# Optimization experiments

Hardware: AMD Instinct MI355X
Metric: run time of the kernel (lower is better)

The kernel has to match this reference:

```python
import jax, jax.numpy as jnp
import numpy as np

D = 256
H = 8
DIM = D // H
NL = 8  # number of layers
LAYER_NAMES = ["self", "cross", "self", "cross", "self", "cross", "self", "cross"]
EPS_ATTN = 1e-6
EPS_LN = 1e-5


def setup_inputs() -> dict:
    key = jax.random.key(0)
    ks = jax.random.split(key, 16)
    B, L = 8, 4800
    s = 1.0 / np.sqrt(D)
    inp = {
        "desc0": jax.random.normal(ks[0], (B, L, D), jnp.float32),
        "desc1": jax.random.normal(ks[1], (B, L, D), jnp.float32),
        "mask0": jnp.ones((B, L), jnp.float32),
        "mask1": jnp.ones((B, L), jnp.float32),
        # shared LinearAttention params (one instance reused by all layers)
        "Wq": jax.random.normal(ks[2], (D, D), jnp.float32) * s,
        "bq": jnp.zeros((D,), jnp.float32),
        "Wk": jax.random.normal(ks[3], (D, D), jnp.float32) * s,
        "bk": jnp.zeros((D,), jnp.float32),
        "Wv": jax.random.normal(ks[4], (D, D), jnp.float32) * s,
        "bv": jnp.zeros((D,), jnp.float32),
        "Wm": jax.random.normal(ks[5], (D, D), jnp.float32) * s,
        "bm": jnp.zeros((D,), jnp.float32),
        # per-layer MLP (no bias) and layernorm params, stacked over layers
        "w1": jax.random.normal(ks[6], (NL, D, 2 * D), jnp.float32) * s,
        "w2": jax.random.normal(ks[7], (NL, 2 * D, D), jnp.float32) * (1.0 / np.sqrt(2 * D)),
        "g1": jnp.ones((NL, D), jnp.float32),
        "b1": jnp.zeros((NL, D), jnp.float32),
        "g2": jnp.ones((NL, D), jnp.float32),
        "b2": jnp.zeros((NL, D), jnp.float32),
    }
    return inp


def _layernorm(x, g, b):
    mu = jnp.mean(x, axis=-1, keepdims=True)
    var = jnp.mean(jnp.square(x - mu), axis=-1, keepdims=True)
    return (x - mu) * jax.lax.rsqrt(var + EPS_LN) * g + b


def _linear_attention(q_in, k_in, v_in, qmask, kmask, Wq, bq, Wk, bk, Wv, bv, Wm, bm):
    B, L, _ = q_in.shape
    Q = (q_in @ Wq + bq).reshape(B, -1, H, DIM)
    K = (k_in @ Wk + bk).reshape(B, -1, H, DIM)
    V = (v_in @ Wv + bv).reshape(B, -1, H, DIM)
    Q = jax.nn.elu(Q) + 1.0
    K = jax.nn.elu(K) + 1.0
    Q = Q * qmask[:, :, None, None]
    K = K * kmask[:, :, None, None]
    V = V * kmask[:, :, None, None]
    KV = jnp.einsum("nshd,nshm->nhmd", K, V)          # [B,H,DIM,DIM]
    Z = 1.0 / (jnp.einsum("nlhd,nhd->nlh", Q, K.sum(axis=1)) + EPS_ATTN)
    out = jnp.einsum("nlhd,nhmd,nlh->nlhm", Q, KV, Z)  # [B,L,H,DIM]
    return out.reshape(B, L, D) @ Wm + bm


def _layer(x, source, xmask, smask, Wq, bq, Wk, bk, Wv, bv, Wm, bm, w1, w2, g1, b1, g2, b2):
    msg = _linear_attention(x, source, source, xmask, smask, Wq, bq, Wk, bk, Wv, bv, Wm, bm)
    msg = _layernorm(msg, g1, b1)
    msg = jax.nn.relu(msg @ w1) @ w2
    msg = _layernorm(msg, g2, b2)
    return x + msg


def reference(desc0, desc1, mask0, mask1, Wq, bq, Wk, bk, Wv, bv, Wm, bm, w1, w2, g1, b1, g2, b2):
    attn = (Wq, bq, Wk, bk, Wv, bv, Wm, bm)
    for i, name in enumerate(LAYER_NAMES):
        lp = (w1[i], w2[i], g1[i], b1[i], g2[i], b2[i])
        if name == "self":
            desc0 = _layer(desc0, desc0, mask0, mask0, *attn, *lp)
            desc1 = _layer(desc1, desc1, mask1, mask1, *attn, *lp)
        else:
            desc0 = _layer(desc0, desc1, mask0, mask1, *attn, *lp)
            desc1 = _layer(desc1, desc0, mask1, mask0, *attn, *lp)
    return (desc0, desc1)
```

## Files before the change

### kernel.cpp

```cpp
#include <hip/hip_runtime.h>
#include <hip/hip_bf16.h>

typedef __attribute__((ext_vector_type(8))) short short8;
typedef __attribute__((ext_vector_type(4))) float f32x4;

#define NROWS 38400
#define LSEQ 4800
#define BATCH 8
#define NHEAD 8
#define QKV_LD 768

__device__ inline float b2f(ushort u) {
  union { ushort s; __hip_bfloat16 h; } c;
  c.s = u;
  return __bfloat162float(c.h);
}
__device__ inline ushort f2b(float f) {
  union { ushort s; __hip_bfloat16 h; } c;
  c.h = __float2bfloat16(f);
  return c.s;
}

__device__ inline void gll16(const void* g, void* l) {
  __builtin_amdgcn_global_load_lds(
      (const __attribute__((address_space(1))) void*)g,
      (__attribute__((address_space(3))) void*)l, 16, 0, 0);
}

__global__ __launch_bounds__(256) void transpose_bf16(
    const float* __restrict__ src, __hip_bfloat16* __restrict__ dst, int R, int C) {
  src += (size_t)blockIdx.z * R * C;
  dst += (size_t)blockIdx.z * R * C;
  __shared__ float tile[32][33];
  int bx = blockIdx.x, by = blockIdx.y;
  int tx = threadIdx.x & 31, ty = threadIdx.x >> 5;
  for (int rr = ty; rr < 32; rr += 8)
    tile[rr][tx] = src[(long)(by * 32 + rr) * C + bx * 32 + tx];
  __syncthreads();
  for (int rr = ty; rr < 32; rr += 8)
    dst[(long)(bx * 32 + rr) * R + by * 32 + tx] = __float2bfloat16(tile[tx][rr]);
}

__global__ __launch_bounds__(256) void init_x(
    const float* __restrict__ d0, const float* __restrict__ d1,
    float* __restrict__ outF, __hip_bfloat16* __restrict__ X0b,
    __hip_bfloat16* __restrict__ X1b, long n4) {
  long i = (long)blockIdx.x * 256 + threadIdx.x;
  if (i < n4) {
    float4 a = ((const float4*)d0)[i];
    float4 b = ((const float4*)d1)[i];
    ((float4*)outF)[i] = a;
    ((float4*)outF)[n4 + i] = b;
    ushort4 ua = {f2b(a.x), f2b(a.y), f2b(a.z), f2b(a.w)};
    ushort4 ub = {f2b(b.x), f2b(b.y), f2b(b.z), f2b(b.w)};
    ((ushort4*)X0b)[i] = ua;
    ((ushort4*)X1b)[i] = ub;
  }
}

__global__ __launch_bounds__(256) void gemm_qkv(
    const __hip_bfloat16* __restrict__ A, const __hip_bfloat16* __restrict__ Bt,
    __hip_bfloat16* __restrict__ C, int col0,
    const float* __restrict__ bq, const float* __restrict__ bk,
    const float* __restrict__ bv, const float* __restrict__ mq,
    const float* __restrict__ mkv) {
  __shared__ alignas(16) char smem[128 * 136 * 2];
  __hip_bfloat16 (*As)[64] = (__hip_bfloat16(*)[64])smem;
  __hip_bfloat16 (*Bs)[64] = (__hip_bfloat16(*)[64])(smem + 128 * 64 * 2);
  ushort (*Cs)[136] = (ushort(*)[136])smem;

  int tid = threadIdx.x;
  int wave = tid >> 6, lane = tid & 63;
  int wm = wave & 1, wn = wave >> 1;
  int quad = lane >> 4, l16 = lane & 15;
  long mbase = (long)blockIdx.y * 128;
  int nbase = blockIdx.x * 128;

  int srow = lane >> 3;
  int sck = (lane & 7) ^ srow;
  int cx = l16 & 7;

  f32x4 acc[4][4];
#pragma unroll
  for (int i = 0; i < 4; i++)
#pragma unroll
    for (int j = 0; j < 4; j++) acc[i][j] = (f32x4){0.f, 0.f, 0.f, 0.f};

  for (int kt = 0; kt < 256; kt += 64) {
    __syncthreads();
#pragma unroll
    for (int i = 0; i < 4; i++) {
      int r0 = wave * 32 + i * 8;
      gll16(A + (mbase + r0 + srow) * 256 + kt + sck * 8, &As[r0][0]);
      gll16(Bt + (long)(nbase + r0 + srow) * 256 + kt + sck * 8, &Bs[r0][0]);
    }
    __syncthreads();
#pragma unroll
    for (int ks = 0; ks < 64; ks += 32) {
      short8 af[4], bfr[4];
      int ch = ((ks >> 3) + quad) ^ cx;
#pragma unroll
      for (int mt = 0; mt < 4; mt++)
        af[mt] = *(const short8*)&As[wm * 64 + mt * 16 + l16][ch * 8];
#pragma unroll
      for (int nt = 0; nt < 4; nt++)
        bfr[nt] = *(const short8*)&Bs[wn * 64 + nt * 16 + l16][ch * 8];
#pragma unroll
      for (int mt = 0; mt < 4; mt++)
#pragma unroll
        for (int nt = 0; nt < 4; nt++)
          acc[mt][nt] = __builtin_amdgcn_mfma_f32_16x16x32_bf16(
              af[mt], bfr[nt], acc[mt][nt], 0, 0, 0);
    }
  }

  __syncthreads();
  int gc0 = col0 + nbase;
#pragma unroll
  for (int nt = 0; nt < 4; nt++) {
    int colt = wn * 64 + nt * 16 + l16;
    int gcol = gc0 + colt;
    int seg = gcol >> 8;
    int ci = gcol & 255;
    float bvv = (seg == 0) ? bq[ci] : (seg == 1) ? bk[ci] : bv[ci];
    const float* mask = (seg == 0) ? mq : mkv;
    bool doelu = seg < 2;
#pragma unroll
    for (int mt = 0; mt < 4; mt++) {
      int rowt0 = wm * 64 + mt * 16 + quad * 4;
#pragma unroll
      for (int r = 0; r < 4; r++) {
        int rowt = rowt0 + r;
        float v = acc[mt][nt][r] + bvv;
        if (doelu) v = v > 0.f ? v + 1.f : __expf(v);
        v *= mask[mbase + rowt];
        Cs[rowt][colt] = f2b(v);
      }
    }
  }
  __syncthreads();
#pragma unroll
  for (int it = 0; it < 8; it++) {
    int idx = tid + it * 256;
    int row = idx >> 4, c = idx & 15;
    uint4 v = *(const uint4*)&Cs[row][c * 8];
    *(uint4*)(C + (mbase + row) * (long)QKV_LD + gc0 + c * 8) = v;
  }
}

__global__ __launch_bounds__(256) void gemm_w1(
    const __hip_bfloat16* __restrict__ A, const __hip_bfloat16* __restrict__ Bt,
    __hip_bfloat16* __restrict__ C) {
  __shared__ alignas(16) char smem[128 * 136 * 2];
  __hip_bfloat16 (*As)[64] = (__hip_bfloat16(*)[64])smem;
  __hip_bfloat16 (*Bs)[64] = (__hip_bfloat16(*)[64])(smem + 128 * 64 * 2);
  ushort (*Cs)[136] = (ushort(*)[136])smem;

  int tid = threadIdx.x;
  int wave = tid >> 6, lane = tid & 63;
  int wm = wave & 1, wn = wave >> 1;
  int quad = lane >> 4, l16 = lane & 15;
  long mbase = (long)blockIdx.y * 128;
  int nbase = blockIdx.x * 128;

  int srow = lane >> 3;
  int sck = (lane & 7) ^ srow;
  int cx = l16 & 7;

  f32x4 acc[4][4];
#pragma unroll
  for (int i = 0; i < 4; i++)
#pragma unroll
    for (int j = 0; j < 4; j++) acc[i][j] = (f32x4){0.f, 0.f, 0.f, 0.f};

  for (int kt = 0; kt < 256; kt += 64) {
    __syncthreads();
#pragma unroll
    for (int i = 0; i < 4; i++) {
      int r0 = wave * 32 + i * 8;
      gll16(A + (mbase + r0 + srow) * 256 + kt + sck * 8, &As[r0][0]);
      gll16(Bt + (long)(nbase + r0 + srow) * 256 + kt + sck * 8, &Bs[r0][0]);
    }
    __syncthreads();
#pragma unroll
    for (int ks = 0; ks < 64; ks += 32) {
      short8 af[4], bfr[4];
      int ch = ((ks >> 3) + quad) ^ cx;
#pragma unroll
      for (int mt = 0; mt < 4; mt++)
        af[mt] = *(const short8*)&As[wm * 64 + mt * 16 + l16][ch * 8];
#pragma unroll
      for (int nt = 0; nt < 4; nt++)
        bfr[nt] = *(const short8*)&Bs[wn * 64 + nt * 16 + l16][ch * 8];
#pragma unroll
      for (int mt = 0; mt < 4; mt++)
#pragma unroll
        for (int nt = 0; nt < 4; nt++)
          acc[mt][nt] = __builtin_amdgcn_mfma_f32_16x16x32_bf16(
              af[mt], bfr[nt], acc[mt][nt], 0, 0, 0);
    }
  }

  __syncthreads();
#pragma unroll
  for (int nt = 0; nt < 4; nt++) {
    int colt = wn * 64 + nt * 16 + l16;
#pragma unroll
    for (int mt = 0; mt < 4; mt++) {
      int rowt0 = wm * 64 + mt * 16 + quad * 4;
#pragma unroll
      for (int r = 0; r < 4; r++) {
        float v = acc[mt][nt][r];
        Cs[rowt0 + r][colt] = f2b(v > 0.f ? v : 0.f);
      }
    }
  }
  __syncthreads();
#pragma unroll
  for (int it = 0; it < 8; it++) {
    int idx = tid + it * 256;
    int row = idx >> 4, c = idx & 15;
    uint4 v = *(const uint4*)&Cs[row][c * 8];
    *(uint4*)(C + (mbase + row) * 512L + nbase + c * 8) = v;
  }
}

__global__ __launch_bounds__(256) void gemm_ln(
    const __hip_bfloat16* __restrict__ A, const __hip_bfloat16* __restrict__ Bt,
    const float* __restrict__ bias, const float* __restrict__ g,
    const float* __restrict__ bln, __hip_bfloat16* __restrict__ C) {
  __shared__ alignas(16) char smem[8192 + 32768];
  __hip_bfloat16 (*As)[64] = (__hip_bfloat16(*)[64])smem;
  __hip_bfloat16 (*Bs)[64] = (__hip_bfloat16(*)[64])(smem + 8192);
  ushort (*Cs)[264] = (ushort(*)[264])smem;
  float* pS  = (float*)(smem + 33792);
  float* pS2 = (float*)(smem + 34816);
  float* muA = (float*)(smem + 35840);
  float* rsA = (float*)(smem + 36096);

  int tid = threadIdx.x;
  int wave = tid >> 6, lane = tid & 63;
  int wn = wave;
  int quad = lane >> 4, l16 = lane & 15;
  long mbase = (long)blockIdx.x * 64;

  int srow = lane >> 3;
  int sck = (lane & 7) ^ srow;
  int cx = l16 & 7;

  f32x4 acc[4][4];
#pragma unroll
  for (int i = 0; i < 4; i++)
#pragma unroll
    for (int j = 0; j < 4; j++) acc[i][j] = (f32x4){0.f, 0.f, 0.f, 0.f};

  for (int kt = 0; kt < 256; kt += 64) {
    __syncthreads();
#pragma unroll
    for (int j = 0; j < 2; j++) {
      int r0 = wave * 16 + j * 8;
      gll16(A + (mbase + r0 + srow) * 256 + kt + sck * 8, &As[r0][0]);
    }
#pragma unroll
    for (int j = 0; j < 8; j++) {
      int r0 = wave * 64 + j * 8;
      gll16(Bt + (r0 + srow) * 256 + kt + sck * 8, &Bs[r0][0]);
    }
    __syncthreads();
#pragma unroll
    for (int ks = 0; ks < 64; ks += 32) {
      short8 af[4], bfr[4];
      int ch = ((ks >> 3) + quad) ^ cx;
#pragma unroll
      for (int mt = 0; mt < 4; mt++)
        af[mt] = *(const short8*)&As[mt * 16 + l16][ch * 8];
#pragma unroll
      for (int nt = 0; nt < 4; nt++)
        bfr[nt] = *(const short8*)&Bs[wn * 64 + nt * 16 + l16][ch * 8];
#pragma unroll
      for (int mt = 0; mt < 4; mt++)
#pragma unroll
        for (int nt = 0; nt < 4; nt++)
          acc[mt][nt] = __builtin_amdgcn_mfma_f32_16x16x32_bf16(
              af[mt], bfr[nt], acc[mt][nt], 0, 0, 0);
    }
  }
  __syncthreads();

  float br[4], gr[4], blr[4];
#pragma unroll
  for (int nt = 0; nt < 4; nt++) {
    int gcol = wn * 64 + nt * 16 + l16;
    br[nt] = bias[gcol];
    gr[nt] = g[gcol];
    blr[nt] = bln[gcol];
  }
#pragma unroll
  for (int mt = 0; mt < 4; mt++)
#pragma unroll
    for (int r = 0; r < 4; r++) {
      float s = 0.f, s2 = 0.f;
#pragma unroll
      for (int nt = 0; nt < 4; nt++) {
        float v = acc[mt][nt][r] + br[nt];
        s += v;
        s2 += v * v;
      }
      s += __shfl_xor(s, 1);  s2 += __shfl_xor(s2, 1);
      s += __shfl_xor(s, 2);  s2 += __shfl_xor(s2, 2);
      s += __shfl_xor(s, 4);  s2 += __shfl_xor(s2, 4);
      s += __shfl_xor(s, 8);  s2 += __shfl_xor(s2, 8);
      if (l16 == 0) {
        int row = mt * 16 + quad * 4 + r;
        pS[wn * 64 + row] = s;
        pS2[wn * 64 + row] = s2;
      }
    }
  __syncthreads();
  if (tid < 64) {
    float S = pS[tid] + pS[64 + tid] + pS[128 + tid] + pS[192 + tid];
    float S2 = pS2[tid] + pS2[64 + tid] + pS2[128 + tid] + pS2[192 + tid];
    float mu = S * (1.f / 256.f);
    float var = S2 * (1.f / 256.f) - mu * mu;
    muA[tid] = mu;
    rsA[tid] = rsqrtf(var + 1e-5f);
  }
  __syncthreads();
#pragma unroll
  for (int mt = 0; mt < 4; mt++)
#pragma unroll
    for (int r = 0; r < 4; r++) {
      int row = mt * 16 + quad * 4 + r;
      float mu = muA[row], rs = rsA[row];
#pragma unroll
      for (int nt = 0; nt < 4; nt++) {
        float v = acc[mt][nt][r] + br[nt];
        Cs[row][wn * 64 + nt * 16 + l16] = f2b((v - mu) * rs * gr[nt] + blr[nt]);
      }
    }
  __syncthreads();
#pragma unroll
  for (int it = 0; it < 8; it++) {
    int idx = tid + it * 256;
    int row = idx >> 5, c = idx & 31;
    uint4 v = *(const uint4*)&Cs[row][c * 8];
    *(uint4*)(C + (mbase + row) * 256L + c * 8) = v;
  }
}

__global__ __launch_bounds__(256) void gemm_final(
    const __hip_bfloat16* __restrict__ A, const __hip_bfloat16* __restrict__ Bt,
    const float* __restrict__ g, const float* __restrict__ bln,
    float* __restrict__ outF, __hip_bfloat16* __restrict__ Xb) {
  __shared__ alignas(16) char smem[8192 + 32768];
  __hip_bfloat16 (*As)[64] = (__hip_bfloat16(*)[64])smem;
  __hip_bfloat16 (*Bs)[64] = (__hip_bfloat16(*)[64])(smem + 8192);
  ushort (*Cs)[264] = (ushort(*)[264])smem;
  float* pS  = (float*)(smem + 33792);
  float* pS2 = (float*)(smem + 34816);
  float* muA = (float*)(smem + 35840);
  float* rsA = (float*)(smem + 36096);

  int tid = threadIdx.x;
  int wave = tid >> 6, lane = tid & 63;
  int wn = wave;
  int quad = lane >> 4, l16 = lane & 15;
  long mbase = (long)blockIdx.x * 64;

  int srow = lane >> 3;
  int sck = (lane & 7) ^ srow;
  int cx = l16 & 7;

  f32x4 acc[4][4];
#pragma unroll
  for (int i = 0; i < 4; i++)
#pragma unroll
    for (int j = 0; j < 4; j++) acc[i][j] = (f32x4){0.f, 0.f, 0.f, 0.f};

  for (int kt = 0; kt < 512; kt += 64) {
    __syncthreads();
#pragma unroll
    for (int j = 0; j < 2; j++) {
      int r0 = wave * 16 + j * 8;
      gll16(A + (mbase + r0 + srow) * 512 + kt + sck * 8, &As[r0][0]);
    }
#pragma unroll
    for (int j = 0; j < 8; j++) {
      int r0 = wave * 64 + j * 8;
      gll16(Bt + (r0 + srow) * 512L + kt + sck * 8, &Bs[r0][0]);
    }
    __syncthreads();
#pragma unroll
    for (int ks = 0; ks < 64; ks += 32) {
      short8 af[4], bfr[4];
      int ch = ((ks >> 3) + quad) ^ cx;
#pragma unroll
      for (int mt = 0; mt < 4; mt++)
        af[mt] = *(const short8*)&As[mt * 16 + l16][ch * 8];
#pragma unroll
      for (int nt = 0; nt < 4; nt++)
        bfr[nt] = *(const short8*)&Bs[wn * 64 + nt * 16 + l16][ch * 8];
#pragma unroll
      for (int mt = 0; mt < 4; mt++)
#pragma unroll
        for (int nt = 0; nt < 4; nt++)
          acc[mt][nt] = __builtin_amdgcn_mfma_f32_16x16x32_bf16(
              af[mt], bfr[nt], acc[mt][nt], 0, 0, 0);
    }
  }
  __syncthreads();

  float gr[4], blr[4];
#pragma unroll
  for (int nt = 0; nt < 4; nt++) {
    int gcol = wn * 64 + nt * 16 + l16;
    gr[nt] = g[gcol];
    blr[nt] = bln[gcol];
  }
#pragma unroll
  for (int mt = 0; mt < 4; mt++)
#pragma unroll
    for (int r = 0; r < 4; r++) {
      float s = 0.f, s2 = 0.f;
#pragma unroll
      for (int nt = 0; nt < 4; nt++) {
        float v = acc[mt][nt][r];
        s += v;
        s2 += v * v;
      }
      s += __shfl_xor(s, 1);  s2 += __shfl_xor(s2, 1);
      s += __shfl_xor(s, 2);  s2 += __shfl_xor(s2, 2);
      s += __shfl_xor(s, 4);  s2 += __shfl_xor(s2, 4);
      s += __shfl_xor(s, 8);  s2 += __shfl_xor(s2, 8);
      if (l16 == 0) {
        int row = mt * 16 + quad * 4 + r;
        pS[wn * 64 + row] = s;
        pS2[wn * 64 + row] = s2;
      }
    }
  __syncthreads();
  if (tid < 64) {
    float S = pS[tid] + pS[64 + tid] + pS[128 + tid] + pS[192 + tid];
    float S2 = pS2[tid] + pS2[64 + tid] + pS2[128 + tid] + pS2[192 + tid];
    float mu = S * (1.f / 256.f);
    float var = S2 * (1.f / 256.f) - mu * mu;
    muA[tid] = mu;
    rsA[tid] = rsqrtf(var + 1e-5f);
  }
  __syncthreads();
#pragma unroll
  for (int mt = 0; mt < 4; mt++)
#pragma unroll
    for (int r = 0; r < 4; r++) {
      int row = mt * 16 + quad * 4 + r;
      float mu = muA[row], rs = rsA[row];
#pragma unroll
      for (int nt = 0; nt < 4; nt++) {
        int gcol = wn * 64 + nt * 16 + l16;
        float ln = (acc[mt][nt][r] - mu) * rs * gr[nt] + blr[nt];
        float* op = outF + (mbase + row) * 256 + gcol;
        float rr = *op + ln;
        *op = rr;
        Cs[row][gcol] = f2b(rr);
      }
    }
  __syncthreads();
#pragma unroll
  for (int it = 0; it < 8; it++) {
    int idx = tid + it * 256;
    int row = idx >> 5, c = idx & 31;
    uint4 v = *(const uint4*)&Cs[row][c * 8];
    *(uint4*)(Xb + (mbase + row) * 256L + c * 8) = v;
  }
}

__global__ __launch_bounds__(256) void kv_reduce(
    const __hip_bfloat16* __restrict__ QKV, float* __restrict__ KV,
    float* __restrict__ Ksum) {
  int b = blockIdx.x, h = blockIdx.y, c = blockIdx.z;
  __shared__ float Kl[32][40], Vl[32][40];
  int t = threadIdx.x;
  int lrow = t >> 3, le = (t & 7) * 4;
  int d = t >> 3, mg = t & 7;
  float a0 = 0.f, a1 = 0.f, a2 = 0.f, a3 = 0.f, ks = 0.f;
  int base = c * 480;
  for (int st = 0; st < 15; st++) {
    int s0 = base + st * 32;
    __syncthreads();
    {
      long n = (long)b * LSEQ + s0 + lrow;
      ushort4 ku = *(const ushort4*)(QKV + n * QKV_LD + 256 + h * 32 + le);
      ushort4 vu = *(const ushort4*)(QKV + n * QKV_LD + 512 + h * 32 + le);
      float4 kf = {b2f(ku.x), b2f(ku.y), b2f(ku.z), b2f(ku.w)};
      float4 vf = {b2f(vu.x), b2f(vu.y), b2f(vu.z), b2f(vu.w)};
      *(float4*)&Kl[lrow][le] = kf;
      *(float4*)&Vl[lrow][le] = vf;
    }
    __syncthreads();
#pragma unroll
    for (int ss = 0; ss < 32; ss++) {
      float kd = Kl[ss][d];
      float4 v4 = *(const float4*)&Vl[ss][mg * 4];
      a0 += kd * v4.x; a1 += kd * v4.y; a2 += kd * v4.z; a3 += kd * v4.w;
      if (mg == 0) ks += kd;
    }
  }
  int bh = b * 8 + h;
  float* p = KV + ((long)bh * 32 + d) * 32 + mg * 4;
  atomicAdd(&p[0], a0); atomicAdd(&p[1], a1);
  atomicAdd(&p[2], a2); atomicAdd(&p[3], a3);
  if (mg == 0) atomicAdd(&Ksum[bh * 32 + d], ks);
}

__global__ __launch_bounds__(256) void attn_out(
    const __hip_bfloat16* __restrict__ QKV, const float* __restrict__ KV,
    const float* __restrict__ Ksum, __hip_bfloat16* __restrict__ O) {
  int b = blockIdx.y, h = blockIdx.z;
  int bh = b * 8 + h;
  __shared__ float KVl[32][36];
  int t = threadIdx.x;
  for (int i = t; i < 1024; i += 256) KVl[i >> 5][i & 31] = KV[((long)bh << 10) + i];
  int lane = t & 63, wave = t >> 6;
  int cg = lane & 7, rs = lane >> 3;
  float4 ksr = *(const float4*)&Ksum[bh * 32 + cg * 4];
  __syncthreads();

  int rowEnd = blockIdx.x * 192 + 192;
  for (int r = blockIdx.x * 192 + wave * 8 + rs; r < rowEnd; r += 32) {
    long n = (long)b * LSEQ + r;
    ushort4 qu = *(const ushort4*)(QKV + n * QKV_LD + h * 32 + cg * 4);
    float q0 = b2f(qu.x), q1 = b2f(qu.y), q2 = b2f(qu.z), q3 = b2f(qu.w);
    float den = q0 * ksr.x + q1 * ksr.y + q2 * ksr.z + q3 * ksr.w;
    den += __shfl_xor(den, 1);
    den += __shfl_xor(den, 2);
    den += __shfl_xor(den, 4);
    float s0 = 0.f, s1 = 0.f, s2 = 0.f, s3 = 0.f;
    int gbase = lane & ~7;
#pragma unroll
    for (int j = 0; j < 8; j++) {
      int src = gbase | j;
      float qa = __shfl(q0, src);
      float qb = __shfl(q1, src);
      float qc = __shfl(q2, src);
      float qd = __shfl(q3, src);
      float4 k0 = *(const float4*)&KVl[j * 4 + 0][cg * 4];
      float4 k1 = *(const float4*)&KVl[j * 4 + 1][cg * 4];
      float4 k2 = *(const float4*)&KVl[j * 4 + 2][cg * 4];
      float4 k3 = *(const float4*)&KVl[j * 4 + 3][cg * 4];
      s0 += qa * k0.x + qb * k1.x + qc * k2.x + qd * k3.x;
      s1 += qa * k0.y + qb * k1.y + qc * k2.y + qd * k3.y;
      s2 += qa * k0.z + qb * k1.z + qc * k2.z + qd * k3.z;
      s3 += qa * k0.w + qb * k1.w + qc * k2.w + qd * k3.w;
    }
    float inv = 1.0f / (den + 1e-6f);
    ushort4 ou = {f2b(s0 * inv), f2b(s1 * inv), f2b(s2 * inv), f2b(s3 * inv)};
    *(ushort4*)(O + n * 256 + h * 32 + cg * 4) = ou;
  }
}

extern "C" void kernel_launch(void* const* d_in, const int* in_sizes, int n_in,
                              void* d_out, int out_size, void* d_ws, size_t ws_size,
                              hipStream_t stream) {
  const float* desc0 = (const float*)d_in[0];
  const float* desc1 = (const float*)d_in[1];
  const float* mask0 = (const float*)d_in[2];
  const float* mask1 = (const float*)d_in[3];
  const float* Wq = (const float*)d_in[4];
  const float* bq = (const float*)d_in[5];
  const float* Wk = (const float*)d_in[6];
  const float* bk = (const float*)d_in[7];
  const float* Wv = (const float*)d_in[8];
  const float* bv = (const float*)d_in[9];
  const float* Wm = (const float*)d_in[10];
  const float* bm = (const float*)d_in[11];
  const float* w1 = (const float*)d_in[12];
  const float* w2 = (const float*)d_in[13];
  const float* g1 = (const float*)d_in[14];
  const float* b1 = (const float*)d_in[15];
  const float* g2 = (const float*)d_in[16];
  const float* b2 = (const float*)d_in[17];

  char* ws = (char*)d_ws;
  size_t used = 0;
  auto alloc = [&](size_t bytes) {
    char* p = ws + used;
    used += (bytes + 255) & ~(size_t)255;
    return p;
  };
  __hip_bfloat16* WqkvT = (__hip_bfloat16*)alloc((size_t)768 * 256 * 2);
  __hip_bfloat16* WmT = (__hip_bfloat16*)alloc(256 * 256 * 2);
  __hip_bfloat16* w1T = (__hip_bfloat16*)alloc((size_t)8 * 512 * 256 * 2);
  __hip_bfloat16* w2T = (__hip_bfloat16*)alloc((size_t)8 * 256 * 512 * 2);
  __hip_bfloat16* X0b = (__hip_bfloat16*)alloc((size_t)NROWS * 256 * 2);
  __hip_bfloat16* X1b = (__hip_bfloat16*)alloc((size_t)NROWS * 256 * 2);
  __hip_bfloat16* QKV = (__hip_bfloat16*)alloc((size_t)NROWS * QKV_LD * 2);
  __hip_bfloat16* Mb2 = QKV;
  __hip_bfloat16* Ab2 = (__hip_bfloat16*)alloc((size_t)2 * NROWS * 256 * 2);
  __hip_bfloat16* H1b2 = (__hip_bfloat16*)alloc((size_t)2 * NROWS * 512 * 2);
  float* KVws = (float*)alloc((64 * 1024 + 64 * 32) * 4);
  float* Ksum = KVws + 64 * 1024;
  bool merged = used <= ws_size;

  transpose_bf16<<<dim3(8, 8, 1), 256, 0, stream>>>(Wq, WqkvT, 256, 256);
  transpose_bf16<<<dim3(8, 8, 1), 256, 0, stream>>>(Wk, WqkvT + 65536, 256, 256);
  transpose_bf16<<<dim3(8, 8, 1), 256, 0, stream>>>(Wv, WqkvT + 131072, 256, 256);
  transpose_bf16<<<dim3(8, 8, 1), 256, 0, stream>>>(Wm, WmT, 256, 256);
  transpose_bf16<<<dim3(16, 8, 8), 256, 0, stream>>>(w1, w1T, 256, 512);
  transpose_bf16<<<dim3(8, 16, 8), 256, 0, stream>>>(w2, w2T, 512, 256);

  long nElem = (long)NROWS * 256;
  long n4 = nElem / 4;
  init_x<<<(n4 + 255) / 256, 256, 0, stream>>>(desc0, desc1, (float*)d_out,
                                               X0b, X1b, n4);

  auto attn_stage = [&](const __hip_bfloat16* Xq, const __hip_bfloat16* Xkv,
                        const float* mq, const float* ms,
                        __hip_bfloat16* Oout, bool self) {
    if (self) {
      gemm_qkv<<<dim3(6, 300), 256, 0, stream>>>(Xq, WqkvT, QKV, 0,
                                                 bq, bk, bv, mq, ms);
    } else {
      gemm_qkv<<<dim3(2, 300), 256, 0, stream>>>(Xq, WqkvT, QKV, 0,
                                                 bq, bk, bv, mq, ms);
      gemm_qkv<<<dim3(4, 300), 256, 0, stream>>>(Xkv, WqkvT + 65536, QKV, 256,
                                                 bq, bk, bv, mq, ms);
    }
    hipMemsetAsync(KVws, 0, (64 * 1024 + 64 * 32) * 4, stream);
    kv_reduce<<<dim3(BATCH, NHEAD, 10), 256, 0, stream>>>(QKV, KVws, Ksum);
    attn_out<<<dim3(25, BATCH, NHEAD), 256, 0, stream>>>(QKV, KVws, Ksum, Oout);
  };

  auto self_pair = [&](int i) {
    attn_stage(X0b, X0b, mask0, mask0, Ab2, true);
    attn_stage(X1b, X1b, mask1, mask1, Ab2 + nElem, true);
    gemm_ln<<<2 * NROWS / 64, 256, 0, stream>>>(Ab2, WmT, bm, g1 + i * 256,
                                                b1 + i * 256, Mb2);
    gemm_w1<<<dim3(4, 2 * NROWS / 128), 256, 0, stream>>>(
        Mb2, w1T + (size_t)i * 512 * 256, H1b2);
    gemm_final<<<2 * NROWS / 64, 256, 0, stream>>>(
        H1b2, w2T + (size_t)i * 256 * 512, g2 + i * 256, b2 + i * 256,
        (float*)d_out, X0b);
  };

  auto layer_one = [&](int x, int s, int i) {
    __hip_bfloat16* Xx = x ? X1b : X0b;
    __hip_bfloat16* Xs = s ? X1b : X0b;
    const float* mx = x ? mask1 : mask0;
    const float* ms = s ? mask1 : mask0;
    attn_stage(Xx, Xs, mx, ms, Ab2, x == s);
    gemm_ln<<<NROWS / 64, 256, 0, stream>>>(Ab2, WmT, bm, g1 + i * 256,
                                            b1 + i * 256, Mb2);
    gemm_w1<<<dim3(4, NROWS / 128), 256, 0, stream>>>(
        Mb2, w1T + (size_t)i * 512 * 256, H1b2);
    gemm_final<<<NROWS / 64, 256, 0, stream>>>(
        H1b2, w2T + (size_t)i * 256 * 512, g2 + i * 256, b2 + i * 256,
        (float*)d_out + (size_t)x * nElem, Xx);
  };

  for (int i = 0; i < 8; i++) {
    if (i % 2 == 0) {
      if (merged) {
        self_pair(i);
      } else {
        layer_one(0, 0, i);
        layer_one(1, 1, i);
      }
    } else {
      layer_one(0, 1, i);
      layer_one(1, 0, i);
    }
  }
}
```

Before: 3.331 ms.

## Double-buffer LDS tiles in gemm_ln and gemm_final to overlap loads with MFMA

The K-loop in gemm_ln and gemm_final now uses two LDS buffers. The next tile is issued with global_load_lds while MFMAs run on the current tile, and only one barrier is kept per iteration. This hides global-to-LDS load latency behind compute. In exchange, LDS use grows to 80KB per block, which may cut how many blocks fit per CU and so lower occupancy.

```diff
diff --git a/kernel.cpp b/kernel.cpp
--- a/kernel.cpp
+++ b/kernel.cpp
@@ -229,9 +229,7 @@
     const __hip_bfloat16* __restrict__ A, const __hip_bfloat16* __restrict__ Bt,
     const float* __restrict__ bias, const float* __restrict__ g,
     const float* __restrict__ bln, __hip_bfloat16* __restrict__ C) {
-  __shared__ alignas(16) char smem[8192 + 32768];
-  __hip_bfloat16 (*As)[64] = (__hip_bfloat16(*)[64])smem;
-  __hip_bfloat16 (*Bs)[64] = (__hip_bfloat16(*)[64])(smem + 8192);
+  __shared__ alignas(16) char smem[81920];
   ushort (*Cs)[264] = (ushort(*)[264])smem;
   float* pS  = (float*)(smem + 33792);
   float* pS2 = (float*)(smem + 34816);
@@ -254,8 +252,10 @@
 #pragma unroll
     for (int j = 0; j < 4; j++) acc[i][j] = (f32x4){0.f, 0.f, 0.f, 0.f};
 
-  for (int kt = 0; kt < 256; kt += 64) {
-    __syncthreads();
+  auto stage = [&](int bi, int kt) {
+    char* base = smem + bi * 40960;
+    __hip_bfloat16 (*As)[64] = (__hip_bfloat16(*)[64])base;
+    __hip_bfloat16 (*Bs)[64] = (__hip_bfloat16(*)[64])(base + 8192);
 #pragma unroll
     for (int j = 0; j < 2; j++) {
       int r0 = wave * 16 + j * 8;
@@ -266,7 +266,11 @@
       int r0 = wave * 64 + j * 8;
       gll16(Bt + (r0 + srow) * 256 + kt + sck * 8, &Bs[r0][0]);
     }
-    __syncthreads();
+  };
+  auto compute = [&](int bi) {
+    char* base = smem + bi * 40960;
+    __hip_bfloat16 (*As)[64] = (__hip_bfloat16(*)[64])base;
+    __hip_bfloat16 (*Bs)[64] = (__hip_bfloat16(*)[64])(base + 8192);
 #pragma unroll
     for (int ks = 0; ks < 64; ks += 32) {
       short8 af[4], bfr[4];
@@ -284,8 +288,20 @@
           acc[mt][nt] = __builtin_amdgcn_mfma_f32_16x16x32_bf16(
               af[mt], bfr[nt], acc[mt][nt], 0, 0, 0);
     }
-  }
-  __syncthreads();
+  };
+
+  stage(0, 0);
+  asm volatile("s_waitcnt vmcnt(0)" ::: "memory");
+  __builtin_amdgcn_sched_barrier(0);
+  __builtin_amdgcn_s_barrier();
+#pragma unroll
+  for (int t = 0; t < 4; t++) {
+    if (t + 1 < 4) stage((t + 1) & 1, (t + 1) * 64);
+    compute(t & 1);
+    asm volatile("s_waitcnt vmcnt(0)" ::: "memory");
+    __builtin_amdgcn_sched_barrier(0);
+    __builtin_amdgcn_s_barrier();
+  }
 
   float br[4], gr[4], blr[4];
 #pragma unroll
@@ -352,9 +368,7 @@
     const __hip_bfloat16* __restrict__ A, const __hip_bfloat16* __restrict__ Bt,
     const float* __restrict__ g, const float* __restrict__ bln,
     float* __restrict__ outF, __hip_bfloat16* __restrict__ Xb) {
-  __shared__ alignas(16) char smem[8192 + 32768];
-  __hip_bfloat16 (*As)[64] = (__hip_bfloat16(*)[64])smem;
-  __hip_bfloat16 (*Bs)[64] = (__hip_bfloat16(*)[64])(smem + 8192);
+  __shared__ alignas(16) char smem[81920];
   ushort (*Cs)[264] = (ushort(*)[264])smem;
   float* pS  = (float*)(smem + 33792);
   float* pS2 = (float*)(smem + 34816);
@@ -377,8 +391,10 @@
 #pragma unroll
     for (int j = 0; j < 4; j++) acc[i][j] = (f32x4){0.f, 0.f, 0.f, 0.f};
 
-  for (int kt = 0; kt < 512; kt += 64) {
-    __syncthreads();
+  auto stage = [&](int bi, int kt) {
+    char* base = smem + bi * 40960;
+    __hip_bfloat16 (*As)[64] = (__hip_bfloat16(*)[64])base;
+    __hip_bfloat16 (*Bs)[64] = (__hip_bfloat16(*)[64])(base + 8192);
 #pragma unroll
     for (int j = 0; j < 2; j++) {
       int r0 = wave * 16 + j * 8;
@@ -389,7 +405,11 @@
       int r0 = wave * 64 + j * 8;
       gll16(Bt + (r0 + srow) * 512L + kt + sck * 8, &Bs[r0][0]);
     }
-    __syncthreads();
+  };
+  auto compute = [&](int bi) {
+    char* base = smem + bi * 40960;
+    __hip_bfloat16 (*As)[64] = (__hip_bfloat16(*)[64])base;
+    __hip_bfloat16 (*Bs)[64] = (__hip_bfloat16(*)[64])(base + 8192);
 #pragma unroll
     for (int ks = 0; ks < 64; ks += 32) {
       short8 af[4], bfr[4];
@@ -407,8 +427,20 @@
           acc[mt][nt] = __builtin_amdgcn_mfma_f32_16x16x32_bf16(
               af[mt], bfr[nt], acc[mt][nt], 0, 0, 0);
     }
-  }
-  __syncthreads();
+  };
+
+  stage(0, 0);
+  asm volatile("s_waitcnt vmcnt(0)" ::: "memory");
+  __builtin_amdgcn_sched_barrier(0);
+  __builtin_amdgcn_s_barrier();
+#pragma unroll
+  for (int t = 0; t < 8; t++) {
+    if (t + 1 < 8) stage((t + 1) & 1, (t + 1) * 64);
+    compute(t & 1);
+    asm volatile("s_waitcnt vmcnt(0)" ::: "memory");
+    __builtin_amdgcn_sched_barrier(0);
+    __builtin_amdgcn_s_barrier();
+  }
 
   float gr[4], blr[4];
 #pragma unroll
```

Result: no change. 3.266 ms (-1.9%).

## Fuse output projection, LayerNorm, MLP and final LayerNorm into one kernel

Applied to the files above, without the earlier changes.

Replaces the three tail kernels (Wm GEMM + LN1, W1 GEMM + ReLU, W2 GEMM + LN2 + residual) with a single 512-thread kernel per 64-row tile. The intermediate M and H1 activations stay in swizzled shared memory instead of round-tripping through global memory. Weight tiles are double-buffered with global_load_lds prefetch of the next stage. This removes launches and large intermediate HBM traffic, at the cost of about 150KB LDS per block (one block per CU) and re-reading all weights for every row tile.

```diff
diff --git a/kernel.cpp b/kernel.cpp
--- a/kernel.cpp
+++ b/kernel.cpp
@@ -148,152 +148,154 @@
   }
 }
 
-__global__ __launch_bounds__(256) void gemm_w1(
-    const __hip_bfloat16* __restrict__ A, const __hip_bfloat16* __restrict__ Bt,
-    __hip_bfloat16* __restrict__ C) {
-  __shared__ alignas(16) char smem[128 * 136 * 2];
-  __hip_bfloat16 (*As)[64] = (__hip_bfloat16(*)[64])smem;
-  __hip_bfloat16 (*Bs)[64] = (__hip_bfloat16(*)[64])(smem + 128 * 64 * 2);
-  ushort (*Cs)[136] = (ushort(*)[136])smem;
+__global__ __launch_bounds__(512) void tail_fused(
+    const __hip_bfloat16* __restrict__ A, const __hip_bfloat16* __restrict__ WmT,
+    const __hip_bfloat16* __restrict__ w1T, const __hip_bfloat16* __restrict__ w2T,
+    const float* __restrict__ bm,
+    const float* __restrict__ g1, const float* __restrict__ b1,
+    const float* __restrict__ g2, const float* __restrict__ b2,
+    float* __restrict__ outF, __hip_bfloat16* __restrict__ Xb) {
+  __shared__ alignas(16) char smem[152064];
+  ushort* Msu  = (ushort*)(smem + 81920);
+  ushort* H1u  = (ushort*)(smem + 114688);
+  float* pS  = (float*)(smem + 147456);
+  float* pS2 = (float*)(smem + 149504);
+  float* muA = (float*)(smem + 151552);
+  float* rsA = (float*)(smem + 151808);
 
   int tid = threadIdx.x;
   int wave = tid >> 6, lane = tid & 63;
-  int wm = wave & 1, wn = wave >> 1;
   int quad = lane >> 4, l16 = lane & 15;
-  long mbase = (long)blockIdx.y * 128;
-  int nbase = blockIdx.x * 128;
-
+  long mbase = (long)blockIdx.x * 64;
   int srow = lane >> 3;
   int sck = (lane & 7) ^ srow;
   int cx = l16 & 7;
-
-  f32x4 acc[4][4];
+  int swz = cx * 8;
+
+  f32x4 accA[4][2], accB[4][2], accC[4][2];
 #pragma unroll
   for (int i = 0; i < 4; i++)
 #pragma unroll
-    for (int j = 0; j < 4; j++) acc[i][j] = (f32x4){0.f, 0.f, 0.f, 0.f};
-
-  for (int kt = 0; kt < 256; kt += 64) {
-    __syncthreads();
-#pragma unroll
-    for (int i = 0; i < 4; i++) {
-      int r0 = wave * 32 + i * 8;
-      gll16(A + (mbase + r0 + srow) * 256 + kt + sck * 8, &As[r0][0]);
-      gll16(Bt + (long)(nbase + r0 + srow) * 256 + kt + sck * 8, &Bs[r0][0]);
-    }
-    __syncthreads();
+    for (int j = 0; j < 2; j++) {
+      accA[i][j] = (f32x4){0.f, 0.f, 0.f, 0.f};
+      accC[i][j] = (f32x4){0.f, 0.f, 0.f, 0.f};
+    }
+
+  auto stageA = [&](int b, int kt) {
+    char* base = smem + b * 40960;
+    __hip_bfloat16 (*As)[64] = (__hip_bfloat16(*)[64])base;
+    __hip_bfloat16 (*Bs)[64] = (__hip_bfloat16(*)[64])(base + 8192);
+    gll16(A + (mbase + wave * 8 + srow) * 256 + kt + sck * 8, &As[wave * 8][0]);
+#pragma unroll
+    for (int j = 0; j < 4; j++) {
+      int r0 = wave * 32 + j * 8;
+      gll16(WmT + (r0 + srow) * 256 + kt + sck * 8, &Bs[r0][0]);
+    }
+  };
+  auto stageB = [&](int b, int half, int kt) {
+    __hip_bfloat16 (*Bs)[64] = (__hip_bfloat16(*)[64])(smem + b * 40960 + 8192);
+#pragma unroll
+    for (int j = 0; j < 4; j++) {
+      int r0 = wave * 32 + j * 8;
+      gll16(w1T + (half * 256 + r0 + srow) * 256 + kt + sck * 8, &Bs[r0][0]);
+    }
+  };
+  auto stageC = [&](int b, int half, int kt) {
+    __hip_bfloat16 (*Bs)[64] = (__hip_bfloat16(*)[64])(smem + b * 40960 + 8192);
+#pragma unroll
+    for (int j = 0; j < 4; j++) {
+      int r0 = wave * 32 + j * 8;
+      gll16(w2T + (r0 + srow) * 512L + half * 256 + kt + sck * 8, &Bs[r0][0]);
+    }
+  };
+
+  auto computeA = [&](int b) {
+    char* base = smem + b * 40960;
+    __hip_bfloat16 (*As)[64] = (__hip_bfloat16(*)[64])base;
+    __hip_bfloat16 (*Bs)[64] = (__hip_bfloat16(*)[64])(base + 8192);
 #pragma unroll
     for (int ks = 0; ks < 64; ks += 32) {
-      short8 af[4], bfr[4];
+      short8 af[4], bfr[2];
       int ch = ((ks >> 3) + quad) ^ cx;
 #pragma unroll
       for (int mt = 0; mt < 4; mt++)
-        af[mt] = *(const short8*)&As[wm * 64 + mt * 16 + l16][ch * 8];
-#pragma unroll
-      for (int nt = 0; nt < 4; nt++)
-        bfr[nt] = *(const short8*)&Bs[wn * 64 + nt * 16 + l16][ch * 8];
-#pragma unroll
-      for (int mt = 0; mt < 4; mt++)
-#pragma unroll
-        for (int nt = 0; nt < 4; nt++)
-          acc[mt][nt] = __builtin_amdgcn_mfma_f32_16x16x32_bf16(
-              af[mt], bfr[nt], acc[mt][nt], 0, 0, 0);
-    }
-  }
-
-  __syncthreads();
-#pragma unroll
-  for (int nt = 0; nt < 4; nt++) {
-    int colt = wn * 64 + nt * 16 + l16;
-#pragma unroll
-    for (int mt = 0; mt < 4; mt++) {
-      int rowt0 = wm * 64 + mt * 16 + quad * 4;
-#pragma unroll
-      for (int r = 0; r < 4; r++) {
-        float v = acc[mt][nt][r];
-        Cs[rowt0 + r][colt] = f2b(v > 0.f ? v : 0.f);
-      }
-    }
-  }
-  __syncthreads();
-#pragma unroll
-  for (int it = 0; it < 8; it++) {
-    int idx = tid + it * 256;
-    int row = idx >> 4, c = idx & 15;
-    uint4 v = *(const uint4*)&Cs[row][c * 8];
-    *(uint4*)(C + (mbase + row) * 512L + nbase + c * 8) = v;
-  }
-}
-
-__global__ __launch_bounds__(256) void gemm_ln(
-    const __hip_bfloat16* __restrict__ A, const __hip_bfloat16* __restrict__ Bt,
-    const float* __restrict__ bias, const float* __restrict__ g,
-    const float* __restrict__ bln, __hip_bfloat16* __restrict__ C) {
-  __shared__ alignas(16) char smem[8192 + 32768];
-  __hip_bfloat16 (*As)[64] = (__hip_bfloat16(*)[64])smem;
-  __hip_bfloat16 (*Bs)[64] = (__hip_bfloat16(*)[64])(smem + 8192);
-  ushort (*Cs)[264] = (ushort(*)[264])smem;
-  float* pS  = (float*)(smem + 33792);
-  float* pS2 = (float*)(smem + 34816);
-  float* muA = (float*)(smem + 35840);
-  float* rsA = (float*)(smem + 36096);
-
-  int tid = threadIdx.x;
-  int wave = tid >> 6, lane = tid & 63;
-  int wn = wave;
-  int quad = lane >> 4, l16 = lane & 15;
-  long mbase = (long)blockIdx.x * 64;
-
-  int srow = lane >> 3;
-  int sck = (lane & 7) ^ srow;
-  int cx = l16 & 7;
-
-  f32x4 acc[4][4];
-#pragma unroll
-  for (int i = 0; i < 4; i++)
-#pragma unroll
-    for (int j = 0; j < 4; j++) acc[i][j] = (f32x4){0.f, 0.f, 0.f, 0.f};
-
-  for (int kt = 0; kt < 256; kt += 64) {
-    __syncthreads();
-#pragma unroll
-    for (int j = 0; j < 2; j++) {
-      int r0 = wave * 16 + j * 8;
-      gll16(A + (mbase + r0 + srow) * 256 + kt + sck * 8, &As[r0][0]);
-    }
-#pragma unroll
-    for (int j = 0; j < 8; j++) {
-      int r0 = wave * 64 + j * 8;
-      gll16(Bt + (r0 + srow) * 256 + kt + sck * 8, &Bs[r0][0]);
-    }
-    __syncthreads();
+        af[mt] = *(const short8*)&As[mt * 16 + l16][ch * 8];
+#pragma unroll
+      for (int nt = 0; nt < 2; nt++)
+        bfr[nt] = *(const short8*)&Bs[wave * 32 + nt * 16 + l16][ch * 8];
+#pragma unroll
+      for (int mt = 0; mt < 4; mt++)
+#pragma unroll
+        for (int nt = 0; nt < 2; nt++)
+          accA[mt][nt] = __builtin_amdgcn_mfma_f32_16x16x32_bf16(
+              af[mt], bfr[nt], accA[mt][nt], 0, 0, 0);
+    }
+  };
+  auto computeB = [&](int b, int kt) {
+    __hip_bfloat16 (*Bs)[64] = (__hip_bfloat16(*)[64])(smem + b * 40960 + 8192);
 #pragma unroll
     for (int ks = 0; ks < 64; ks += 32) {
-      short8 af[4], bfr[4];
+      short8 af[4], bfr[2];
       int ch = ((ks >> 3) + quad) ^ cx;
-#pragma unroll
-      for (int mt = 0; mt < 4; mt++)
-        af[mt] = *(const short8*)&As[mt * 16 + l16][ch * 8];
-#pragma unroll
-      for (int nt = 0; nt < 4; nt++)
-        bfr[nt] = *(const short8*)&Bs[wn * 64 + nt * 16 + l16][ch * 8];
-#pragma unroll
-      for (int mt = 0; mt < 4; mt++)
-#pragma unroll
-        for (int nt = 0; nt < 4; nt++)
-          acc[mt][nt] = __builtin_amdgcn_mfma_f32_16x16x32_bf16(
-              af[mt], bfr[nt], acc[mt][nt], 0, 0, 0);
-    }
-  }
-  __syncthreads();
-
-  float br[4], gr[4], blr[4];
-#pragma unroll
-  for (int nt = 0; nt < 4; nt++) {
-    int gcol = wn * 64 + nt * 16 + l16;
-    br[nt] = bias[gcol];
-    gr[nt] = g[gcol];
-    blr[nt] = bln[gcol];
+      int mcol = (kt + ks + quad * 8) ^ swz;
+#pragma unroll
+      for (int mt = 0; mt < 4; mt++)
+        af[mt] = *(const short8*)&Msu[(mt * 16 + l16) * 256 + mcol];
+#pragma unroll
+      for (int nt = 0; nt < 2; nt++)
+        bfr[nt] = *(const short8*)&Bs[wave * 32 + nt * 16 + l16][ch * 8];
+#pragma unroll
+      for (int mt = 0; mt < 4; mt++)
+#pragma unroll
+        for (int nt = 0; nt < 2; nt++)
+          accB[mt][nt] = __builtin_amdgcn_mfma_f32_16x16x32_bf16(
+              af[mt], bfr[nt], accB[mt][nt], 0, 0, 0);
+    }
+  };
+  auto computeC = [&](int b, int kt) {
+    __hip_bfloat16 (*Bs)[64] = (__hip_bfloat16(*)[64])(smem + b * 40960 + 8192);
+#pragma unroll
+    for (int ks = 0; ks < 64; ks += 32) {
+      short8 af[4], bfr[2];
+      int ch = ((ks >> 3) + quad) ^ cx;
+      int hcol = (kt + ks + quad * 8) ^ swz;
+#pragma unroll
+      for (int mt = 0; mt < 4; mt++)
+        af[mt] = *(const short8*)&H1u[(mt * 16 + l16) * 256 + hcol];
+#pragma unroll
+      for (int nt = 0; nt < 2; nt++)
+        bfr[nt] = *(const short8*)&Bs[wave * 32 + nt * 16 + l16][ch * 8];
+#pragma unroll
+      for (int mt = 0; mt < 4; mt++)
+#pragma unroll
+        for (int nt = 0; nt < 2; nt++)
+          accC[mt][nt] = __builtin_amdgcn_mfma_f32_16x16x32_bf16(
+              af[mt], bfr[nt], accC[mt][nt], 0, 0, 0);
+    }
+  };
+
+#define PIPE_SYNC                                      \
+  asm volatile("s_waitcnt vmcnt(0)" ::: "memory");     \
+  __builtin_amdgcn_sched_barrier(0);                   \
+  __builtin_amdgcn_s_barrier();
+
+  int cb = 0;
+  stageA(0, 0);
+  PIPE_SYNC
+#pragma unroll
+  for (int t = 0; t < 4; t++) {
+    if (t < 3) stageA(cb ^ 1, (t + 1) * 64); else stageB(cb ^ 1, 0, 0);
+    computeA(cb);
+    PIPE_SYNC
+    cb ^= 1;
+  }
+  float br[2], gr[2], blr[2];
+#pragma unroll
+  for (int nt = 0; nt < 2; nt++) {
+    int gcol = wave * 32 + nt * 16 + l16;
+    br[nt] = bm[gcol];
+    gr[nt] = g1[gcol];
+    blr[nt] = b1[gcol];
   }
 #pragma unroll
   for (int mt = 0; mt < 4; mt++)
@@ -301,8 +303,8 @@
     for (int r = 0; r < 4; r++) {
       float s = 0.f, s2 = 0.f;
 #pragma unroll
-      for (int nt = 0; nt < 4; nt++) {
-        float v = acc[mt][nt][r] + br[nt];
+      for (int nt = 0; nt < 2; nt++) {
+        float v = accA[mt][nt][r] + br[nt];
         s += v;
         s2 += v * v;
       }
@@ -312,14 +314,15 @@
       s += __shfl_xor(s, 8);  s2 += __shfl_xor(s2, 8);
       if (l16 == 0) {
         int row = mt * 16 + quad * 4 + r;
-        pS[wn * 64 + row] = s;
-        pS2[wn * 64 + row] = s2;
+        pS[wave * 64 + row] = s;
+        pS2[wave * 64 + row] = s2;
       }
     }
   __syncthreads();
   if (tid < 64) {
-    float S = pS[tid] + pS[64 + tid] + pS[128 + tid] + pS[192 + tid];
-    float S2 = pS2[tid] + pS2[64 + tid] + pS2[128 + tid] + pS2[192 + tid];
+    float S = 0.f, S2 = 0.f;
+#pragma unroll
+    for (int w = 0; w < 8; w++) { S += pS[w * 64 + tid]; S2 += pS2[w * 64 + tid]; }
     float mu = S * (1.f / 256.f);
     float var = S2 * (1.f / 256.f) - mu * mu;
     muA[tid] = mu;
@@ -332,90 +335,59 @@
     for (int r = 0; r < 4; r++) {
       int row = mt * 16 + quad * 4 + r;
       float mu = muA[row], rs = rsA[row];
-#pragma unroll
-      for (int nt = 0; nt < 4; nt++) {
-        float v = acc[mt][nt][r] + br[nt];
-        Cs[row][wn * 64 + nt * 16 + l16] = f2b((v - mu) * rs * gr[nt] + blr[nt]);
-      }
-    }
-  __syncthreads();
-#pragma unroll
-  for (int it = 0; it < 8; it++) {
-    int idx = tid + it * 256;
-    int row = idx >> 5, c = idx & 31;
-    uint4 v = *(const uint4*)&Cs[row][c * 8];
-    *(uint4*)(C + (mbase + row) * 256L + c * 8) = v;
-  }
-}
-
-__global__ __launch_bounds__(256) void gemm_final(
-    const __hip_bfloat16* __restrict__ A, const __hip_bfloat16* __restrict__ Bt,
-    const float* __restrict__ g, const float* __restrict__ bln,
-    float* __restrict__ outF, __hip_bfloat16* __restrict__ Xb) {
-  __shared__ alignas(16) char smem[8192 + 32768];
-  __hip_bfloat16 (*As)[64] = (__hip_bfloat16(*)[64])smem;
-  __hip_bfloat16 (*Bs)[64] = (__hip_bfloat16(*)[64])(smem + 8192);
-  ushort (*Cs)[264] = (ushort(*)[264])smem;
-  float* pS  = (float*)(smem + 33792);
-  float* pS2 = (float*)(smem + 34816);
-  float* muA = (float*)(smem + 35840);
-  float* rsA = (float*)(smem + 36096);
-
-  int tid = threadIdx.x;
-  int wave = tid >> 6, lane = tid & 63;
-  int wn = wave;
-  int quad = lane >> 4, l16 = lane & 15;
-  long mbase = (long)blockIdx.x * 64;
-
-  int srow = lane >> 3;
-  int sck = (lane & 7) ^ srow;
-  int cx = l16 & 7;
-
-  f32x4 acc[4][4];
-#pragma unroll
-  for (int i = 0; i < 4; i++)
-#pragma unroll
-    for (int j = 0; j < 4; j++) acc[i][j] = (f32x4){0.f, 0.f, 0.f, 0.f};
-
-  for (int kt = 0; kt < 512; kt += 64) {
+      int rsw = (row & 7) * 8;
+#pragma unroll
+      for (int nt = 0; nt < 2; nt++) {
+        int col = wave * 32 + nt * 16 + l16;
+        float v = accA[mt][nt][r] + br[nt];
+        Msu[row * 256 + (col ^ rsw)] = f2b((v - mu) * rs * gr[nt] + blr[nt]);
+      }
+    }
+  __syncthreads();
+
+#pragma unroll
+  for (int half = 0; half < 2; half++) {
+#pragma unroll
+    for (int i = 0; i < 4; i++)
+#pragma unroll
+      for (int j = 0; j < 2; j++) accB[i][j] = (f32x4){0.f, 0.f, 0.f, 0.f};
+#pragma unroll
+    for (int t = 0; t < 4; t++) {
+      if (t < 3) stageB(cb ^ 1, half, (t + 1) * 64); else stageC(cb ^ 1, half, 0);
+      computeB(cb, t * 64);
+      PIPE_SYNC
+      cb ^= 1;
+    }
+#pragma unroll
+    for (int mt = 0; mt < 4; mt++)
+#pragma unroll
+      for (int r = 0; r < 4; r++) {
+        int row = mt * 16 + quad * 4 + r;
+        int rsw = (row & 7) * 8;
+#pragma unroll
+        for (int nt = 0; nt < 2; nt++) {
+          int col = wave * 32 + nt * 16 + l16;
+          float v = accB[mt][nt][r];
+          H1u[row * 256 + (col ^ rsw)] = f2b(v > 0.f ? v : 0.f);
+        }
+      }
     __syncthreads();
 #pragma unroll
-    for (int j = 0; j < 2; j++) {
-      int r0 = wave * 16 + j * 8;
-      gll16(A + (mbase + r0 + srow) * 512 + kt + sck * 8, &As[r0][0]);
-    }
-#pragma unroll
-    for (int j = 0; j < 8; j++) {
-      int r0 = wave * 64 + j * 8;
-      gll16(Bt + (r0 + srow) * 512L + kt + sck * 8, &Bs[r0][0]);
-    }
-    __syncthreads();
-#pragma unroll
-    for (int ks = 0; ks < 64; ks += 32) {
-      short8 af[4], bfr[4];
-      int ch = ((ks >> 3) + quad) ^ cx;
-#pragma unroll
-      for (int mt = 0; mt < 4; mt++)
-        af[mt] = *(const short8*)&As[mt * 16 + l16][ch * 8];
-#pragma unroll
-      for (int nt = 0; nt < 4; nt++)
-        bfr[nt] = *(const short8*)&Bs[wn * 64 + nt * 16 + l16][ch * 8];
-#pragma unroll
-      for (int mt = 0; mt < 4; mt++)
-#pragma unroll
-        for (int nt = 0; nt < 4; nt++)
-          acc[mt][nt] = __builtin_amdgcn_mfma_f32_16x16x32_bf16(
-              af[mt], bfr[nt], acc[mt][nt], 0, 0, 0);
-    }
-  }
-  __syncthreads();
-
-  float gr[4], blr[4];
-#pragma unroll
-  for (int nt = 0; nt < 4; nt++) {
-    int gcol = wn * 64 + nt * 16 + l16;
-    gr[nt] = g[gcol];
-    blr[nt] = bln[gcol];
+    for (int t = 0; t < 4; t++) {
+      if (t < 3) stageC(cb ^ 1, half, (t + 1) * 64);
+      else if (half == 0) stageB(cb ^ 1, 1, 0);
+      computeC(cb, t * 64);
+      PIPE_SYNC
+      cb ^= 1;
+    }
+  }
+
+  float g2r[2], b2r[2];
+#pragma unroll
+  for (int nt = 0; nt < 2; nt++) {
+    int gcol = wave * 32 + nt * 16 + l16;
+    g2r[nt] = g2[gcol];
+    b2r[nt] = b2[gcol];
   }
 #pragma unroll
   for (int mt = 0; mt < 4; mt++)
@@ -423,8 +395,8 @@
     for (int r = 0; r < 4; r++) {
       float s = 0.f, s2 = 0.f;
 #pragma unroll
-      for (int nt = 0; nt < 4; nt++) {
-        float v = acc[mt][nt][r];
+      for (int nt = 0; nt < 2; nt++) {
+        float v = accC[mt][nt][r];
         s += v;
         s2 += v * v;
       }
@@ -434,20 +406,22 @@
       s += __shfl_xor(s, 8);  s2 += __shfl_xor(s2, 8);
       if (l16 == 0) {
         int row = mt * 16 + quad * 4 + r;
-        pS[wn * 64 + row] = s;
-        pS2[wn * 64 + row] = s2;
+        pS[wave * 64 + row] = s;
+        pS2[wave * 64 + row] = s2;
       }
     }
   __syncthreads();
   if (tid < 64) {
-    float S = pS[tid] + pS[64 + tid] + pS[128 + tid] + pS[192 + tid];
-    float S2 = pS2[tid] + pS2[64 + tid] + pS2[128 + tid] + pS2[192 + tid];
+    float S = 0.f, S2 = 0.f;
+#pragma unroll
+    for (int w = 0; w < 8; w++) { S += pS[w * 64 + tid]; S2 += pS2[w * 64 + tid]; }
     float mu = S * (1.f / 256.f);
     float var = S2 * (1.f / 256.f) - mu * mu;
     muA[tid] = mu;
     rsA[tid] = rsqrtf(var + 1e-5f);
   }
   __syncthreads();
+  ushort* Xsu = Msu;
 #pragma unroll
   for (int mt = 0; mt < 4; mt++)
 #pragma unroll
@@ -455,23 +429,24 @@
       int row = mt * 16 + quad * 4 + r;
       float mu = muA[row], rs = rsA[row];
 #pragma unroll
-      for (int nt = 0; nt < 4; nt++) {
-        int gcol = wn * 64 + nt * 16 + l16;
-        float ln = (acc[mt][nt][r] - mu) * rs * gr[nt] + blr[nt];
+      for (int nt = 0; nt < 2; nt++) {
+        int gcol = wave * 32 + nt * 16 + l16;
+        float ln = (accC[mt][nt][r] - mu) * rs * g2r[nt] + b2r[nt];
         float* op = outF + (mbase + row) * 256 + gcol;
         float rr = *op + ln;
         *op = rr;
-        Cs[row][gcol] = f2b(rr);
-      }
-    }
-  __syncthreads();
-#pragma unroll
-  for (int it = 0; it < 8; it++) {
-    int idx = tid + it * 256;
+        Xsu[row * 256 + gcol] = f2b(rr);
+      }
+    }
+  __syncthreads();
+#pragma unroll
+  for (int it = 0; it < 4; it++) {
+    int idx = tid + it * 512;
     int row = idx >> 5, c = idx & 31;
-    uint4 v = *(const uint4*)&Cs[row][c * 8];
+    uint4 v = *(const uint4*)&Xsu[row * 256 + c * 8];
     *(uint4*)(Xb + (mbase + row) * 256L + c * 8) = v;
   }
+#undef PIPE_SYNC
 }
 
 __global__ __launch_bounds__(256) void kv_reduce(
@@ -594,9 +569,7 @@
   __hip_bfloat16* X0b = (__hip_bfloat16*)alloc((size_t)NROWS * 256 * 2);
   __hip_bfloat16* X1b = (__hip_bfloat16*)alloc((size_t)NROWS * 256 * 2);
   __hip_bfloat16* QKV = (__hip_bfloat16*)alloc((size_t)NROWS * QKV_LD * 2);
-  __hip_bfloat16* Mb2 = QKV;
   __hip_bfloat16* Ab2 = (__hip_bfloat16*)alloc((size_t)2 * NROWS * 256 * 2);
-  __hip_bfloat16* H1b2 = (__hip_bfloat16*)alloc((size_t)2 * NROWS * 512 * 2);
   float* KVws = (float*)alloc((64 * 1024 + 64 * 32) * 4);
   float* Ksum = KVws + 64 * 1024;
   bool merged = used <= ws_size;
@@ -630,16 +603,16 @@
     attn_out<<<dim3(25, BATCH, NHEAD), 256, 0, stream>>>(QKV, KVws, Ksum, Oout);
   };
 
+  auto tail = [&](int nblk, int i, float* oF, __hip_bfloat16* Xb) {
+    tail_fused<<<nblk, 512, 0, stream>>>(
+        Ab2, WmT, w1T + (size_t)i * 512 * 256, w2T + (size_t)i * 256 * 512,
+        bm, g1 + i * 256, b1 + i * 256, g2 + i * 256, b2 + i * 256, oF, Xb);
+  };
+
   auto self_pair = [&](int i) {
     attn_stage(X0b, X0b, mask0, mask0, Ab2, true);
     attn_stage(X1b, X1b, mask1, mask1, Ab2 + nElem, true);
-    gemm_ln<<<2 * NROWS / 64, 256, 0, stream>>>(Ab2, WmT, bm, g1 + i * 256,
-                                                b1 + i * 256, Mb2);
-    gemm_w1<<<dim3(4, 2 * NROWS / 128), 256, 0, stream>>>(
-        Mb2, w1T + (size_t)i * 512 * 256, H1b2);
-    gemm_final<<<2 * NROWS / 64, 256, 0, stream>>>(
-        H1b2, w2T + (size_t)i * 256 * 512, g2 + i * 256, b2 + i * 256,
-        (float*)d_out, X0b);
+    tail(2 * NROWS / 64, i, (float*)d_out, X0b);
   };
 
   auto layer_one = [&](int x, int s, int i) {
@@ -648,13 +621,7 @@
     const float* mx = x ? mask1 : mask0;
     const float* ms = s ? mask1 : mask0;
     attn_stage(Xx, Xs, mx, ms, Ab2, x == s);
-    gemm_ln<<<NROWS / 64, 256, 0, stream>>>(Ab2, WmT, bm, g1 + i * 256,
-                                            b1 + i * 256, Mb2);
-    gemm_w1<<<dim3(4, NROWS / 128), 256, 0, stream>>>(
-        Mb2, w1T + (size_t)i * 512 * 256, H1b2);
-    gemm_final<<<NROWS / 64, 256, 0, stream>>>(
-        H1b2, w2T + (size_t)i * 256 * 512, g2 + i * 256, b2 + i * 256,
-        (float*)d_out + (size_t)x * nElem, Xx);
+    tail(NROWS / 64, i, (float*)d_out + (size_t)x * nElem, Xx);
   };
 
   for (int i = 0; i < 8; i++) {
```

Measured after the change: 3.071 ms. 7.8% less time.
